# Optimization experiments

Hardware: AMD Instinct MI355X
Metric: run time of the kernel (lower is better)

## Reference

```python
import jax, jax.numpy as jnp
import numpy as np

B, N, D, H = 4, 2048, 1024, 64

def setup_inputs() -> dict:
    key = jax.random.key(0)
    ks = jax.random.split(key, 7)
    s = D ** -0.5  # torch Linear default init scale ~ U(-1/sqrt(fan_in), ...); scale randn similarly
    return {
        "x":  jax.random.normal(ks[0], (B, N, D), dtype=jnp.float32),
        "Wq": jax.random.normal(ks[1], (D, H), dtype=jnp.float32) * s,
        "bq": jax.random.normal(ks[2], (H,), dtype=jnp.float32) * s,
        "Wk": jax.random.normal(ks[3], (D, H), dtype=jnp.float32) * s,
        "bk": jax.random.normal(ks[4], (H,), dtype=jnp.float32) * s,
        "Wv": jax.random.normal(ks[5], (D, H), dtype=jnp.float32) * s,
        "bv": jax.random.normal(ks[6], (H,), dtype=jnp.float32) * s,
    }

def reference(x, Wq, bq, Wk, bk, Wv, bv):
    head_size = Wq.shape[1]
    q = x @ Wq + bq          # [B, N, H]
    k = x @ Wk + bk          # [B, N, H]
    v = x @ Wv + bv          # [B, N, H]
    scores = jnp.einsum("bid,bjd->bij", q, k)        # [B, N, N]
    # faithful to torch: keep upper triangle (col >= row), then mask exact zeros to -inf
    scores = jnp.triu(scores)
    scores = jnp.where(scores == 0, -jnp.inf, scores)
    attn = jax.nn.softmax(scores * (head_size ** -0.5), axis=-1)  # [B, N, N]
    # out = (V^T @ attn)^T  ==  attn^T @ V
    out = jnp.einsum("bji,bjh->bih", attn, v)         # [B, N, H]
    return out
```

## Files before the change

### kernel.cpp

```cpp
#include <hip/hip_runtime.h>
#include <math.h>

constexpr int kN = 2048;
constexpr int kD = 1024;

typedef __attribute__((ext_vector_type(8))) short bf16x8;
typedef __attribute__((ext_vector_type(4))) short bf16x4;
typedef __attribute__((ext_vector_type(4))) float f32x4;

#define MFMA(a, b, c) __builtin_amdgcn_mfma_f32_16x16x32_bf16(a, b, c, 0, 0, 0)

__device__ __forceinline__ short f2bf(float f) {
    unsigned u = __float_as_uint(f);
    u += 0x7fff + ((u >> 16) & 1);
    return (short)(u >> 16);
}
__device__ __forceinline__ float bf2f(short s) {
    return __uint_as_float(((unsigned)(unsigned short)s) << 16);
}

__device__ __forceinline__ void g2l(void* lds, const void* g, int nbytes, int t) {
    int lane = t & 63, w = t >> 6;
    for (int base = w * 1024; base < nbytes; base += 4096) {
        if (base + lane * 16 < nbytes) {
            __builtin_amdgcn_global_load_lds(
                (const __attribute__((address_space(1))) void*)((const char*)g + base + lane * 16),
                (__attribute__((address_space(3))) void*)((char*)lds + base),
                16, 0, 0);
        }
    }
}

__global__ __launch_bounds__(256) void prep_kernel(
        const float* __restrict__ Wq, const float* __restrict__ Wk,
        const float* __restrict__ Wv, const float* __restrict__ bq,
        const float* __restrict__ bk, const float* __restrict__ bv,
        short* __restrict__ Wt, float* __restrict__ bcat)
{
    int tid = blockIdx.x * 256 + threadIdx.x;
    int stride = gridDim.x * 256;
    for (int e = tid; e < 16 * 12 * 2 * 512; e += stride) {
        int kc = e / 12288;
        int rem = e - kc * 12288;
        int nt = rem >> 10;
        int r2 = rem & 1023;
        int f = r2 >> 9;
        int r3 = r2 & 511;
        int q8 = r3 >> 7;
        int l15 = (r3 >> 3) & 15;
        int el = r3 & 7;
        int n = nt * 16 + l15;
        int d = kc * 64 + f * 32 + q8 * 8 + el;
        float wv = (n < 64) ? Wq[d * 64 + n]
                 : (n < 128) ? Wk[d * 64 + (n - 64)]
                 : Wv[d * 64 + (n - 128)];
        Wt[e] = f2bf(wv);
    }
    if (tid < 192)
        bcat[tid] = (tid < 64) ? bq[tid] : (tid < 128) ? bk[tid - 64] : bv[tid - 128];
}

constexpr int XP = 1032;

__global__ __launch_bounds__(256) void qkv_kernel(
        const float* __restrict__ x, const short* __restrict__ Wt,
        const float* __restrict__ bcat,
        short* __restrict__ gq, short* __restrict__ gk, short* __restrict__ vt)
{
    __shared__ __align__(16) short xs[16 * XP];
    const int t = threadIdx.x;
    const int w = t >> 6, lane = t & 63, l15 = lane & 15, q8 = lane >> 4;
    const int m0 = blockIdx.x * 16;

    {
        int row = t >> 4, c4 = (t & 15) * 4;
        const float* xr = x + (size_t)(m0 + row) * kD;
        #pragma unroll
        for (int cc = 0; cc < 16; ++cc) {
            float4 xv = *(const float4*)&xr[cc * 64 + c4];
            bf16x4 pk = {f2bf(xv.x), f2bf(xv.y), f2bf(xv.z), f2bf(xv.w)};
            *(bf16x4*)&xs[row * XP + cc * 64 + c4] = pk;
        }
    }
    __syncthreads();

    f32x4 acc[3];
    #pragma unroll
    for (int ct = 0; ct < 3; ++ct) acc[ct] = (f32x4){0.f, 0.f, 0.f, 0.f};

    #pragma unroll 4
    for (int kc = 0; kc < 16; ++kc) {
        bf16x8 a0 = *(const bf16x8*)&xs[l15 * XP + kc * 64 + q8 * 8];
        bf16x8 a1 = *(const bf16x8*)&xs[l15 * XP + kc * 64 + 32 + q8 * 8];
        #pragma unroll
        for (int ct = 0; ct < 3; ++ct) {
            int nt = w * 3 + ct;
            const short* bp = Wt + ((size_t)(kc * 12 + nt) * 2) * 512 + lane * 8;
            bf16x8 b0 = *(const bf16x8*)bp;
            bf16x8 b1 = *(const bf16x8*)(bp + 512);
            acc[ct] = MFMA(a0, b0, acc[ct]);
            acc[ct] = MFMA(a1, b1, acc[ct]);
        }
    }

    const int bz = m0 >> 11;
    const int jt = (m0 & 2047) >> 6;
    const int jb = m0 & 63;
    #pragma unroll
    for (int ct = 0; ct < 3; ++ct) {
        int nb2 = w * 48 + ct * 16;
        int n = nb2 + l15;
        float bias = bcat[n];
        if (nb2 < 64) {
            #pragma unroll
            for (int r = 0; r < 4; ++r)
                gq[(size_t)(m0 + q8 * 4 + r) * 72 + n] = f2bf(acc[ct][r] + bias);
        } else if (nb2 < 128) {
            #pragma unroll
            for (int r = 0; r < 4; ++r)
                gk[(size_t)(m0 + q8 * 4 + r) * 72 + (n - 64)] = f2bf(acc[ct][r] + bias);
        } else {
            int h = n - 128;
            bf16x4 pk = {f2bf(acc[ct][0] + bias), f2bf(acc[ct][1] + bias),
                         f2bf(acc[ct][2] + bias), f2bf(acc[ct][3] + bias)};
            *(bf16x4*)&vt[((size_t)((bz * 32 + jt) * 64 + h)) * 72 + jb + q8 * 4] = pk;
        }
    }
}

__global__ __launch_bounds__(256) void stats_kernel(
        const short* __restrict__ gq, const short* __restrict__ gk,
        float* __restrict__ l2)
{
    __shared__ __align__(16) short qsm[64 * 72];
    __shared__ __align__(16) short ksm[2][64 * 72];
    const int t = threadIdx.x;
    const int w = t >> 6, lane = t & 63, l15 = lane & 15, q8 = lane >> 4;
    const int b = blockIdx.x;
    const int ic = b & 3, bz = (b >> 2) & 3, jt = b >> 4;
    const int j0 = jt * 64;
    const int ilo = ic * 512, ihi = ilo + 512;
    const int istart = (j0 > ilo) ? j0 : ilo;
    const int count = (istart < ihi) ? ((ihi - istart) >> 6) : 0;

    float lloc[4] = {0.f, 0.f, 0.f, 0.f};

    if (count > 0) {
        g2l(qsm, gq + (size_t)(bz * kN + j0) * 72, 64 * 144, t);
        g2l(ksm[0], gk + (size_t)(bz * kN + istart) * 72, 64 * 144, t);
        __syncthreads();
        int jrow = 16 * w + l15;
        bf16x8 a0 = *(const bf16x8*)&qsm[jrow * 72 + q8 * 8];
        bf16x8 a1 = *(const bf16x8*)&qsm[jrow * 72 + 32 + q8 * 8];

        for (int idx = 0; idx < count; ++idx) {
            const int cur = idx & 1;
            if (idx + 1 < count)
                g2l(ksm[cur ^ 1],
                    gk + (size_t)(bz * kN + istart + (idx + 1) * 64) * 72, 64 * 144, t);
            const int i0 = istart + idx * 64;
            #pragma unroll
            for (int it = 0; it < 4; ++it) {
                int irow = it * 16 + l15;
                bf16x8 b0 = *(const bf16x8*)&ksm[cur][irow * 72 + q8 * 8];
                bf16x8 b1 = *(const bf16x8*)&ksm[cur][irow * 72 + 32 + q8 * 8];
                f32x4 s = (f32x4){0.f, 0.f, 0.f, 0.f};
                s = MFMA(a0, b0, s);
                s = MFMA(a1, b1, s);
                int ig = i0 + it * 16 + l15;
                #pragma unroll
                for (int r = 0; r < 4; ++r) {
                    int jg = j0 + 16 * w + q8 * 4 + r;
                    float sv = s[r];
                    float e = __expf(sv * 0.125f);
                    lloc[r] += ((ig >= jg) && (sv != 0.0f)) ? e : 0.0f;
                }
            }
            __syncthreads();
        }
    }
    #pragma unroll
    for (int off = 1; off < 16; off <<= 1)
        #pragma unroll
        for (int r = 0; r < 4; ++r)
            lloc[r] += __shfl_xor(lloc[r], off);
    if (l15 == 0) {
        #pragma unroll
        for (int r = 0; r < 4; ++r)
            l2[ic * 8192 + bz * kN + j0 + 16 * w + q8 * 4 + r] = lloc[r];
    }
}

__global__ __launch_bounds__(256) void vscale_kernel(
        short* __restrict__ vt, const float* __restrict__ l2)
{
    __shared__ float rsm[64];
    const int g = blockIdx.x, t = threadIdx.x;
    if (t < 64) {
        int j = (g >> 5) * kN + (g & 31) * 64 + t;
        float l = l2[j] + l2[8192 + j] + l2[16384 + j] + l2[24576 + j];
        rsm[t] = (l > 0.f) ? 1.0f / l : 0.0f;
    }
    __syncthreads();
    const int h = t >> 2, c0 = (t & 3) * 16;
    size_t base = ((size_t)g * 64 + h) * 72 + c0;
    #pragma unroll
    for (int bb = 0; bb < 2; ++bb) {
        bf16x8 v = *(bf16x8*)&vt[base + bb * 8];
        bf16x8 o;
        #pragma unroll
        for (int e = 0; e < 8; ++e)
            o[e] = f2bf(bf2f(v[e]) * rsm[c0 + bb * 8 + e]);
        *(bf16x8*)&vt[base + bb * 8] = o;
    }
}

__global__ __launch_bounds__(256) void out_kernel(
        const short* __restrict__ gq, const short* __restrict__ gk,
        const short* __restrict__ vt, float* __restrict__ part)
{
    __shared__ __align__(16) short ksm[64 * 72];
    __shared__ __align__(16) short qsm[2][64 * 72];
    __shared__ __align__(16) short vsm[2][64 * 72];
    __shared__ __align__(16) short psm[64 * 72];
    const int t = threadIdx.x;
    const int w = t >> 6, lane = t & 63, l15 = lane & 15, q8 = lane >> 4;
    const int b = blockIdx.x;
    const int jc = b & 3, bz = (b >> 2) & 3, it = b >> 4;
    const int i0 = it * 64;
    const int jlo = jc * 512;
    const int jhi = (jlo + 512 < i0 + 64) ? (jlo + 512) : (i0 + 64);
    const int count = (jlo < jhi) ? ((jhi - jlo) >> 6) : 0;

    f32x4 oacc[4];
    #pragma unroll
    for (int i = 0; i < 4; ++i) oacc[i] = (f32x4){0.f, 0.f, 0.f, 0.f};

    if (count > 0) {
        g2l(ksm, gk + (size_t)(bz * kN + i0) * 72, 64 * 144, t);
        g2l(qsm[0], gq + (size_t)(bz * kN + jlo) * 72, 64 * 144, t);
        g2l(vsm[0], vt + (size_t)((bz * 32 + (jlo >> 6)) * 64) * 72, 64 * 144, t);
        __syncthreads();

        for (int idx = 0; idx < count; ++idx) {
            const int cur = idx & 1, nb = cur ^ 1;
            const int j0s = jlo + idx * 64;
            if (idx + 1 < count) {
                g2l(qsm[nb], gq + (size_t)(bz * kN + j0s + 64) * 72, 64 * 144, t);
                g2l(vsm[nb], vt + (size_t)((bz * 32 + ((j0s + 64) >> 6)) * 64) * 72,
                    64 * 144, t);
            }
            int jrow = 16 * w + l15;
            bf16x8 a0 = *(const bf16x8*)&qsm[cur][jrow * 72 + q8 * 8];
            bf16x8 a1 = *(const bf16x8*)&qsm[cur][jrow * 72 + 32 + q8 * 8];
            #pragma unroll
            for (int itile = 0; itile < 4; ++itile) {
                int irow = itile * 16 + l15;
                bf16x8 b0 = *(const bf16x8*)&ksm[irow * 72 + q8 * 8];
                bf16x8 b1 = *(const bf16x8*)&ksm[irow * 72 + 32 + q8 * 8];
                f32x4 sv4 = (f32x4){0.f, 0.f, 0.f, 0.f};
                sv4 = MFMA(a0, b0, sv4);
                sv4 = MFMA(a1, b1, sv4);
                int ig = i0 + itile * 16 + l15;
                bf16x4 pk;
                #pragma unroll
                for (int r = 0; r < 4; ++r) {
                    int jg = j0s + 16 * w + q8 * 4 + r;
                    float sv = sv4[r];
                    float p = ((ig >= jg) && (sv != 0.0f)) ? __expf(sv * 0.125f) : 0.0f;
                    pk[r] = f2bf(p);
                }
                *(bf16x4*)&psm[(itile * 16 + l15) * 72 + 16 * w + q8 * 4] = pk;
            }
            __syncthreads();

            bf16x8 pa0 = *(const bf16x8*)&psm[(16 * w + l15) * 72 + q8 * 8];
            bf16x8 pa1 = *(const bf16x8*)&psm[(16 * w + l15) * 72 + 32 + q8 * 8];
            #pragma unroll
            for (int ht = 0; ht < 4; ++ht) {
                int vrow = ht * 16 + l15;
                bf16x8 vb0 = *(const bf16x8*)&vsm[cur][vrow * 72 + q8 * 8];
                bf16x8 vb1 = *(const bf16x8*)&vsm[cur][vrow * 72 + 32 + q8 * 8];
                oacc[ht] = MFMA(pa0, vb0, oacc[ht]);
                oacc[ht] = MFMA(pa1, vb1, oacc[ht]);
            }
            __syncthreads();
        }
    }
    size_t base = ((size_t)(jc * 4 + bz) * kN + i0) * 64;
    #pragma unroll
    for (int ht = 0; ht < 4; ++ht)
        #pragma unroll
        for (int r = 0; r < 4; ++r)
            part[base + (size_t)(16 * w + q8 * 4 + r) * 64 + ht * 16 + l15] = oacc[ht][r];
}

__global__ __launch_bounds__(256) void reduce_kernel(
        const float* __restrict__ part, float* __restrict__ out)
{
    int idx = blockIdx.x * 256 + threadIdx.x;
    const float4* p = (const float4*)part;
    float4 a = p[idx];
    float4 b = p[idx + 131072];
    float4 c = p[idx + 262144];
    float4 d = p[idx + 393216];
    float4 r;
    r.x = a.x + b.x + c.x + d.x;
    r.y = a.y + b.y + c.y + d.y;
    r.z = a.z + b.z + c.z + d.z;
    r.w = a.w + b.w + c.w + d.w;
    ((float4*)out)[idx] = r;
}

extern "C" void kernel_launch(void* const* d_in, const int* in_sizes, int n_in,
                              void* d_out, int out_size, void* d_ws, size_t ws_size,
                              hipStream_t stream)
{
    const float* x  = (const float*)d_in[0];
    const float* Wq = (const float*)d_in[1];
    const float* bq = (const float*)d_in[2];
    const float* Wk = (const float*)d_in[3];
    const float* bk = (const float*)d_in[4];
    const float* Wv = (const float*)d_in[5];
    const float* bv = (const float*)d_in[6];
    float* out = (float*)d_out;

    char* base = (char*)d_ws;
    short* Wt   = (short*)(base);
    float* bcat = (float*)(base + 393216);
    short* gq   = (short*)(base + 394240);
    short* gk   = (short*)(base + 1573888);
    short* vt   = (short*)(base + 2753536);
    float* l2   = (float*)(base + 3933184);
    float* part = (float*)(base + 4064256);

    prep_kernel<<<256, 256, 0, stream>>>(Wq, Wk, Wv, bq, bk, bv, Wt, bcat);
    qkv_kernel<<<512, 256, 0, stream>>>(x, Wt, bcat, gq, gk, vt);
    stats_kernel<<<512, 256, 0, stream>>>(gq, gk, l2);
    vscale_kernel<<<128, 256, 0, stream>>>(vt, l2);
    out_kernel<<<512, 256, 0, stream>>>(gq, gk, vt, part);
    reduce_kernel<<<512, 256, 0, stream>>>(part, out);
}
```

Measured before the change: 126.3 us.

## Materialize exp scores in stats pass and reuse them in output pass

The stats kernel now writes the masked exponentiated scores as bf16 into a global buffer, laid out in MFMA-fragment order. The output kernel reads these fragments instead of recomputing QK^T and exp. V is stored in a fragment-friendly tiled layout so it can be loaded straight into registers without LDS or barriers. This removes the duplicated score MFMAs, exp work and LDS staging, but adds about 33 MB of global writes and reads for the P matrix.

```diff
diff --git a/kernel.cpp b/kernel.cpp
--- a/kernel.cpp
+++ b/kernel.cpp
@@ -120,17 +120,23 @@
             for (int r = 0; r < 4; ++r)
                 gk[(size_t)(m0 + q8 * 4 + r) * 72 + (n - 64)] = f2bf(acc[ct][r] + bias);
         } else {
-            int h = n - 128;
+            int ht = (nb2 - 128) >> 4;
+            int base_j = jb + q8 * 4;
+            int f = base_j >> 5;
+            int q8f = (base_j >> 3) & 3;
+            int e0 = base_j & 7;
             bf16x4 pk = {f2bf(acc[ct][0] + bias), f2bf(acc[ct][1] + bias),
                          f2bf(acc[ct][2] + bias), f2bf(acc[ct][3] + bias)};
-            *(bf16x4*)&vt[((size_t)((bz * 32 + jt) * 64 + h)) * 72 + jb + q8 * 4] = pk;
+            size_t addr = (((size_t)((bz * 32 + jt) * 4 + ht) * 2 + f) * 512)
+                          + (q8f * 16 + l15) * 8 + e0;
+            *(bf16x4*)&vt[addr] = pk;
         }
     }
 }
 
 __global__ __launch_bounds__(256) void stats_kernel(
         const short* __restrict__ gq, const short* __restrict__ gk,
-        float* __restrict__ l2)
+        float* __restrict__ l2, short* __restrict__ Pm)
 {
     __shared__ __align__(16) short qsm[64 * 72];
     __shared__ __align__(16) short ksm[2][64 * 72];
@@ -159,6 +165,8 @@
                 g2l(ksm[cur ^ 1],
                     gk + (size_t)(bz * kN + istart + (idx + 1) * 64) * 72, 64 * 144, t);
             const int i0 = istart + idx * 64;
+            const size_t tbase =
+                (((size_t)(bz * 32 + jt) * 32 + (size_t)(i0 >> 6)) * 4 + w) * 4 * 256;
             #pragma unroll
             for (int it = 0; it < 4; ++it) {
                 int irow = it * 16 + l15;
@@ -168,13 +176,17 @@
                 s = MFMA(a0, b0, s);
                 s = MFMA(a1, b1, s);
                 int ig = i0 + it * 16 + l15;
+                bf16x4 pk;
                 #pragma unroll
                 for (int r = 0; r < 4; ++r) {
                     int jg = j0 + 16 * w + q8 * 4 + r;
                     float sv = s[r];
                     float e = __expf(sv * 0.125f);
-                    lloc[r] += ((ig >= jg) && (sv != 0.0f)) ? e : 0.0f;
+                    bool valid = (ig >= jg) && (sv != 0.0f);
+                    lloc[r] += valid ? e : 0.0f;
+                    pk[r] = valid ? f2bf(e) : (short)0;
                 }
+                *(bf16x4*)&Pm[tbase + it * 256 + lane * 4] = pk;
             }
             __syncthreads();
         }
@@ -202,27 +214,29 @@
         rsm[t] = (l > 0.f) ? 1.0f / l : 0.0f;
     }
     __syncthreads();
-    const int h = t >> 2, c0 = (t & 3) * 16;
-    size_t base = ((size_t)g * 64 + h) * 72 + c0;
-    #pragma unroll
-    for (int bb = 0; bb < 2; ++bb) {
-        bf16x8 v = *(bf16x8*)&vt[base + bb * 8];
+    const int slice = t >> 5;
+    const int lane32 = t & 31;
+    const int f = slice & 1;
+    #pragma unroll
+    for (int half = 0; half < 2; ++half) {
+        int lidx = lane32 + half * 32;
+        int q8v = lidx >> 4;
+        size_t addr = ((size_t)g * 8 + slice) * 512 + lidx * 8;
+        bf16x8 v = *(bf16x8*)&vt[addr];
         bf16x8 o;
         #pragma unroll
-        for (int e = 0; e < 8; ++e)
-            o[e] = f2bf(bf2f(v[e]) * rsm[c0 + bb * 8 + e]);
-        *(bf16x8*)&vt[base + bb * 8] = o;
+        for (int e = 0; e < 8; ++e) {
+            int jl = f * 32 + q8v * 8 + e;
+            o[e] = f2bf(bf2f(v[e]) * rsm[jl]);
+        }
+        *(bf16x8*)&vt[addr] = o;
     }
 }
 
 __global__ __launch_bounds__(256) void out_kernel(
-        const short* __restrict__ gq, const short* __restrict__ gk,
-        const short* __restrict__ vt, float* __restrict__ part)
-{
-    __shared__ __align__(16) short ksm[64 * 72];
-    __shared__ __align__(16) short qsm[2][64 * 72];
-    __shared__ __align__(16) short vsm[2][64 * 72];
-    __shared__ __align__(16) short psm[64 * 72];
+        const short* __restrict__ Pm, const short* __restrict__ vt,
+        float* __restrict__ part)
+{
     const int t = threadIdx.x;
     const int w = t >> 6, lane = t & 63, l15 = lane & 15, q8 = lane >> 4;
     const int b = blockIdx.x;
@@ -236,55 +250,26 @@
     #pragma unroll
     for (int i = 0; i < 4; ++i) oacc[i] = (f32x4){0.f, 0.f, 0.f, 0.f};
 
-    if (count > 0) {
-        g2l(ksm, gk + (size_t)(bz * kN + i0) * 72, 64 * 144, t);
-        g2l(qsm[0], gq + (size_t)(bz * kN + jlo) * 72, 64 * 144, t);
-        g2l(vsm[0], vt + (size_t)((bz * 32 + (jlo >> 6)) * 64) * 72, 64 * 144, t);
-        __syncthreads();
-
-        for (int idx = 0; idx < count; ++idx) {
-            const int cur = idx & 1, nb = cur ^ 1;
-            const int j0s = jlo + idx * 64;
-            if (idx + 1 < count) {
-                g2l(qsm[nb], gq + (size_t)(bz * kN + j0s + 64) * 72, 64 * 144, t);
-                g2l(vsm[nb], vt + (size_t)((bz * 32 + ((j0s + 64) >> 6)) * 64) * 72,
-                    64 * 144, t);
-            }
-            int jrow = 16 * w + l15;
-            bf16x8 a0 = *(const bf16x8*)&qsm[cur][jrow * 72 + q8 * 8];
-            bf16x8 a1 = *(const bf16x8*)&qsm[cur][jrow * 72 + 32 + q8 * 8];
-            #pragma unroll
-            for (int itile = 0; itile < 4; ++itile) {
-                int irow = itile * 16 + l15;
-                bf16x8 b0 = *(const bf16x8*)&ksm[irow * 72 + q8 * 8];
-                bf16x8 b1 = *(const bf16x8*)&ksm[irow * 72 + 32 + q8 * 8];
-                f32x4 sv4 = (f32x4){0.f, 0.f, 0.f, 0.f};
-                sv4 = MFMA(a0, b0, sv4);
-                sv4 = MFMA(a1, b1, sv4);
-                int ig = i0 + itile * 16 + l15;
-                bf16x4 pk;
-                #pragma unroll
-                for (int r = 0; r < 4; ++r) {
-                    int jg = j0s + 16 * w + q8 * 4 + r;
-                    float sv = sv4[r];
-                    float p = ((ig >= jg) && (sv != 0.0f)) ? __expf(sv * 0.125f) : 0.0f;
-                    pk[r] = f2bf(p);
-                }
-                *(bf16x4*)&psm[(itile * 16 + l15) * 72 + 16 * w + q8 * 4] = pk;
-            }
-            __syncthreads();
-
-            bf16x8 pa0 = *(const bf16x8*)&psm[(16 * w + l15) * 72 + q8 * 8];
-            bf16x8 pa1 = *(const bf16x8*)&psm[(16 * w + l15) * 72 + 32 + q8 * 8];
-            #pragma unroll
-            for (int ht = 0; ht < 4; ++ht) {
-                int vrow = ht * 16 + l15;
-                bf16x8 vb0 = *(const bf16x8*)&vsm[cur][vrow * 72 + q8 * 8];
-                bf16x8 vb1 = *(const bf16x8*)&vsm[cur][vrow * 72 + 32 + q8 * 8];
-                oacc[ht] = MFMA(pa0, vb0, oacc[ht]);
-                oacc[ht] = MFMA(pa1, vb1, oacc[ht]);
-            }
-            __syncthreads();
+    const int aoff = ((q8 >> 1) * 4 + w) * 256 + (q8 & 1) * 128 + l15 * 4;
+
+    for (int idx = 0; idx < count; ++idx) {
+        const int jt = (jlo >> 6) + idx;
+        const size_t tb = ((size_t)(bz * 32 + jt) * 32 + it) * 16 * 256;
+        const short* pa = Pm + tb + aoff;
+        bf16x4 a00 = *(const bf16x4*)pa;
+        bf16x4 a01 = *(const bf16x4*)(pa + 64);
+        bf16x4 a10 = *(const bf16x4*)(pa + 2048);
+        bf16x4 a11 = *(const bf16x4*)(pa + 2048 + 64);
+        bf16x8 a0 = {a00[0], a00[1], a00[2], a00[3], a01[0], a01[1], a01[2], a01[3]};
+        bf16x8 a1 = {a10[0], a10[1], a10[2], a10[3], a11[0], a11[1], a11[2], a11[3]};
+
+        const short* vb = vt + (size_t)(bz * 32 + jt) * 8 * 512 + lane * 8;
+        #pragma unroll
+        for (int ht = 0; ht < 4; ++ht) {
+            bf16x8 b0 = *(const bf16x8*)(vb + (ht * 2 + 0) * 512);
+            bf16x8 b1 = *(const bf16x8*)(vb + (ht * 2 + 1) * 512);
+            oacc[ht] = MFMA(a0, b0, oacc[ht]);
+            oacc[ht] = MFMA(a1, b1, oacc[ht]);
         }
     }
     size_t base = ((size_t)(jc * 4 + bz) * kN + i0) * 64;
@@ -331,13 +316,14 @@
     short* gq   = (short*)(base + 394240);
     short* gk   = (short*)(base + 1573888);
     short* vt   = (short*)(base + 2753536);
-    float* l2   = (float*)(base + 3933184);
-    float* part = (float*)(base + 4064256);
+    float* l2   = (float*)(base + 3802112);
+    short* Pm   = (short*)(base + 3933184);
+    float* part = (float*)(base + 37487616);
 
     prep_kernel<<<256, 256, 0, stream>>>(Wq, Wk, Wv, bq, bk, bv, Wt, bcat);
     qkv_kernel<<<512, 256, 0, stream>>>(x, Wt, bcat, gq, gk, vt);
-    stats_kernel<<<512, 256, 0, stream>>>(gq, gk, l2);
+    stats_kernel<<<512, 256, 0, stream>>>(gq, gk, l2, Pm);
     vscale_kernel<<<128, 256, 0, stream>>>(vt, l2);
-    out_kernel<<<512, 256, 0, stream>>>(gq, gk, vt, part);
+    out_kernel<<<512, 256, 0, stream>>>(Pm, vt, part);
     reduce_kernel<<<512, 256, 0, stream>>>(part, out);
 }
```

Measured after the change: 127.7 us. About the same (+1.1%).

## Fold V normalization into out_kernel and replace partial reduce with atomics

Applied to the files above, without the earlier changes.

Removes the separate vscale kernel by computing reciprocal column sums in out_kernel and applying them to the probabilities before the PV matmul. Drops the partial-sum buffer and reduce kernel: the output is zeroed in prep_kernel and each j-chunk block atomically adds its contribution. This cuts two launches and the partial-buffer round trip. In exchange it adds float atomics, which make the summation order nondeterministic, and a small per-tile l2 load.

```diff
diff --git a/kernel.cpp b/kernel.cpp
--- a/kernel.cpp
+++ b/kernel.cpp
@@ -14,9 +14,6 @@
     unsigned u = __float_as_uint(f);
     u += 0x7fff + ((u >> 16) & 1);
     return (short)(u >> 16);
-}
-__device__ __forceinline__ float bf2f(short s) {
-    return __uint_as_float(((unsigned)(unsigned short)s) << 16);
 }
 
 __device__ __forceinline__ void g2l(void* lds, const void* g, int nbytes, int t) {
@@ -35,10 +32,13 @@
         const float* __restrict__ Wq, const float* __restrict__ Wk,
         const float* __restrict__ Wv, const float* __restrict__ bq,
         const float* __restrict__ bk, const float* __restrict__ bv,
-        short* __restrict__ Wt, float* __restrict__ bcat)
+        short* __restrict__ Wt, float* __restrict__ bcat,
+        float* __restrict__ out)
 {
     int tid = blockIdx.x * 256 + threadIdx.x;
     int stride = gridDim.x * 256;
+    for (int e = tid; e < 131072; e += stride)
+        ((float4*)out)[e] = make_float4(0.f, 0.f, 0.f, 0.f);
     for (int e = tid; e < 16 * 12 * 2 * 512; e += stride) {
         int kc = e / 12288;
         int rem = e - kc * 12288;
@@ -191,38 +191,16 @@
     }
 }
 
-__global__ __launch_bounds__(256) void vscale_kernel(
-        short* __restrict__ vt, const float* __restrict__ l2)
-{
-    __shared__ float rsm[64];
-    const int g = blockIdx.x, t = threadIdx.x;
-    if (t < 64) {
-        int j = (g >> 5) * kN + (g & 31) * 64 + t;
-        float l = l2[j] + l2[8192 + j] + l2[16384 + j] + l2[24576 + j];
-        rsm[t] = (l > 0.f) ? 1.0f / l : 0.0f;
-    }
-    __syncthreads();
-    const int h = t >> 2, c0 = (t & 3) * 16;
-    size_t base = ((size_t)g * 64 + h) * 72 + c0;
-    #pragma unroll
-    for (int bb = 0; bb < 2; ++bb) {
-        bf16x8 v = *(bf16x8*)&vt[base + bb * 8];
-        bf16x8 o;
-        #pragma unroll
-        for (int e = 0; e < 8; ++e)
-            o[e] = f2bf(bf2f(v[e]) * rsm[c0 + bb * 8 + e]);
-        *(bf16x8*)&vt[base + bb * 8] = o;
-    }
-}
-
 __global__ __launch_bounds__(256) void out_kernel(
         const short* __restrict__ gq, const short* __restrict__ gk,
-        const short* __restrict__ vt, float* __restrict__ part)
+        const short* __restrict__ vt, const float* __restrict__ l2,
+        float* __restrict__ out)
 {
     __shared__ __align__(16) short ksm[64 * 72];
     __shared__ __align__(16) short qsm[2][64 * 72];
     __shared__ __align__(16) short vsm[2][64 * 72];
     __shared__ __align__(16) short psm[64 * 72];
+    __shared__ float rsm[2][64];
     const int t = threadIdx.x;
     const int w = t >> 6, lane = t & 63, l15 = lane & 15, q8 = lane >> 4;
     const int b = blockIdx.x;
@@ -232,84 +210,81 @@
     const int jhi = (jlo + 512 < i0 + 64) ? (jlo + 512) : (i0 + 64);
     const int count = (jlo < jhi) ? ((jhi - jlo) >> 6) : 0;
 
+    if (count <= 0) return;
+
     f32x4 oacc[4];
     #pragma unroll
     for (int i = 0; i < 4; ++i) oacc[i] = (f32x4){0.f, 0.f, 0.f, 0.f};
 
-    if (count > 0) {
-        g2l(ksm, gk + (size_t)(bz * kN + i0) * 72, 64 * 144, t);
-        g2l(qsm[0], gq + (size_t)(bz * kN + jlo) * 72, 64 * 144, t);
-        g2l(vsm[0], vt + (size_t)((bz * 32 + (jlo >> 6)) * 64) * 72, 64 * 144, t);
+    g2l(ksm, gk + (size_t)(bz * kN + i0) * 72, 64 * 144, t);
+    g2l(qsm[0], gq + (size_t)(bz * kN + jlo) * 72, 64 * 144, t);
+    g2l(vsm[0], vt + (size_t)((bz * 32 + (jlo >> 6)) * 64) * 72, 64 * 144, t);
+    if (t < 64) {
+        int j = bz * kN + jlo + t;
+        float l = l2[j] + l2[8192 + j] + l2[16384 + j] + l2[24576 + j];
+        rsm[0][t] = (l > 0.f) ? 1.0f / l : 0.0f;
+    }
+    __syncthreads();
+
+    for (int idx = 0; idx < count; ++idx) {
+        const int cur = idx & 1, nb = cur ^ 1;
+        const int j0s = jlo + idx * 64;
+        if (idx + 1 < count) {
+            g2l(qsm[nb], gq + (size_t)(bz * kN + j0s + 64) * 72, 64 * 144, t);
+            g2l(vsm[nb], vt + (size_t)((bz * 32 + ((j0s + 64) >> 6)) * 64) * 72,
+                64 * 144, t);
+            if (t < 64) {
+                int j = bz * kN + j0s + 64 + t;
+                float l = l2[j] + l2[8192 + j] + l2[16384 + j] + l2[24576 + j];
+                rsm[nb][t] = (l > 0.f) ? 1.0f / l : 0.0f;
+            }
+        }
+        int jrow = 16 * w + l15;
+        bf16x8 a0 = *(const bf16x8*)&qsm[cur][jrow * 72 + q8 * 8];
+        bf16x8 a1 = *(const bf16x8*)&qsm[cur][jrow * 72 + 32 + q8 * 8];
+        #pragma unroll
+        for (int itile = 0; itile < 4; ++itile) {
+            int irow = itile * 16 + l15;
+            bf16x8 b0 = *(const bf16x8*)&ksm[irow * 72 + q8 * 8];
+            bf16x8 b1 = *(const bf16x8*)&ksm[irow * 72 + 32 + q8 * 8];
+            f32x4 sv4 = (f32x4){0.f, 0.f, 0.f, 0.f};
+            sv4 = MFMA(a0, b0, sv4);
+            sv4 = MFMA(a1, b1, sv4);
+            int ig = i0 + itile * 16 + l15;
+            bf16x4 pk;
+            #pragma unroll
+            for (int r = 0; r < 4; ++r) {
+                int jl = 16 * w + q8 * 4 + r;
+                int jg = j0s + jl;
+                float sv = sv4[r];
+                float p = ((ig >= jg) && (sv != 0.0f))
+                        ? __expf(sv * 0.125f) * rsm[cur][jl] : 0.0f;
+                pk[r] = f2bf(p);
+            }
+            *(bf16x4*)&psm[(itile * 16 + l15) * 72 + 16 * w + q8 * 4] = pk;
+        }
         __syncthreads();
 
-        for (int idx = 0; idx < count; ++idx) {
-            const int cur = idx & 1, nb = cur ^ 1;
-            const int j0s = jlo + idx * 64;
-            if (idx + 1 < count) {
-                g2l(qsm[nb], gq + (size_t)(bz * kN + j0s + 64) * 72, 64 * 144, t);
-                g2l(vsm[nb], vt + (size_t)((bz * 32 + ((j0s + 64) >> 6)) * 64) * 72,
-                    64 * 144, t);
-            }
-            int jrow = 16 * w + l15;
-            bf16x8 a0 = *(const bf16x8*)&qsm[cur][jrow * 72 + q8 * 8];
-            bf16x8 a1 = *(const bf16x8*)&qsm[cur][jrow * 72 + 32 + q8 * 8];
-            #pragma unroll
-            for (int itile = 0; itile < 4; ++itile) {
-                int irow = itile * 16 + l15;
-                bf16x8 b0 = *(const bf16x8*)&ksm[irow * 72 + q8 * 8];
-                bf16x8 b1 = *(const bf16x8*)&ksm[irow * 72 + 32 + q8 * 8];
-                f32x4 sv4 = (f32x4){0.f, 0.f, 0.f, 0.f};
-                sv4 = MFMA(a0, b0, sv4);
-                sv4 = MFMA(a1, b1, sv4);
-                int ig = i0 + itile * 16 + l15;
-                bf16x4 pk;
-                #pragma unroll
-                for (int r = 0; r < 4; ++r) {
-                    int jg = j0s + 16 * w + q8 * 4 + r;
-                    float sv = sv4[r];
-                    float p = ((ig >= jg) && (sv != 0.0f)) ? __expf(sv * 0.125f) : 0.0f;
-                    pk[r] = f2bf(p);
-                }
-                *(bf16x4*)&psm[(itile * 16 + l15) * 72 + 16 * w + q8 * 4] = pk;
-            }
-            __syncthreads();
-
-            bf16x8 pa0 = *(const bf16x8*)&psm[(16 * w + l15) * 72 + q8 * 8];
-            bf16x8 pa1 = *(const bf16x8*)&psm[(16 * w + l15) * 72 + 32 + q8 * 8];
-            #pragma unroll
-            for (int ht = 0; ht < 4; ++ht) {
-                int vrow = ht * 16 + l15;
-                bf16x8 vb0 = *(const bf16x8*)&vsm[cur][vrow * 72 + q8 * 8];
-                bf16x8 vb1 = *(const bf16x8*)&vsm[cur][vrow * 72 + 32 + q8 * 8];
-                oacc[ht] = MFMA(pa0, vb0, oacc[ht]);
-                oacc[ht] = MFMA(pa1, vb1, oacc[ht]);
-            }
-            __syncthreads();
-        }
-    }
-    size_t base = ((size_t)(jc * 4 + bz) * kN + i0) * 64;
+        bf16x8 pa0 = *(const bf16x8*)&psm[(16 * w + l15) * 72 + q8 * 8];
+        bf16x8 pa1 = *(const bf16x8*)&psm[(16 * w + l15) * 72 + 32 + q8 * 8];
+        #pragma unroll
+        for (int ht = 0; ht < 4; ++ht) {
+            int vrow = ht * 16 + l15;
+            bf16x8 vb0 = *(const bf16x8*)&vsm[cur][vrow * 72 + q8 * 8];
+            bf16x8 vb1 = *(const bf16x8*)&vsm[cur][vrow * 72 + 32 + q8 * 8];
+            oacc[ht] = MFMA(pa0, vb0, oacc[ht]);
+            oacc[ht] = MFMA(pa1, vb1, oacc[ht]);
+        }
+        __syncthreads();
+    }
+
+    size_t base = ((size_t)(bz * kN + i0)) * 64;
     #pragma unroll
     for (int ht = 0; ht < 4; ++ht)
         #pragma unroll
         for (int r = 0; r < 4; ++r)
-            part[base + (size_t)(16 * w + q8 * 4 + r) * 64 + ht * 16 + l15] = oacc[ht][r];
-}
-
-__global__ __launch_bounds__(256) void reduce_kernel(
-        const float* __restrict__ part, float* __restrict__ out)
-{
-    int idx = blockIdx.x * 256 + threadIdx.x;
-    const float4* p = (const float4*)part;
-    float4 a = p[idx];
-    float4 b = p[idx + 131072];
-    float4 c = p[idx + 262144];
-    float4 d = p[idx + 393216];
-    float4 r;
-    r.x = a.x + b.x + c.x + d.x;
-    r.y = a.y + b.y + c.y + d.y;
-    r.z = a.z + b.z + c.z + d.z;
-    r.w = a.w + b.w + c.w + d.w;
-    ((float4*)out)[idx] = r;
+            atomicAdd(&out[base + (size_t)(16 * w + q8 * 4 + r) * 64 + ht * 16 + l15],
+                      oacc[ht][r]);
 }
 
 extern "C" void kernel_launch(void* const* d_in, const int* in_sizes, int n_in,
@@ -332,12 +307,9 @@
     short* gk   = (short*)(base + 1573888);
     short* vt   = (short*)(base + 2753536);
     float* l2   = (float*)(base + 3933184);
-    float* part = (float*)(base + 4064256);
-
-    prep_kernel<<<256, 256, 0, stream>>>(Wq, Wk, Wv, bq, bk, bv, Wt, bcat);
+
+    prep_kernel<<<256, 256, 0, stream>>>(Wq, Wk, Wv, bq, bk, bv, Wt, bcat, out);
     qkv_kernel<<<512, 256, 0, stream>>>(x, Wt, bcat, gq, gk, vt);
     stats_kernel<<<512, 256, 0, stream>>>(gq, gk, l2);
-    vscale_kernel<<<128, 256, 0, stream>>>(vt, l2);
-    out_kernel<<<512, 256, 0, stream>>>(gq, gk, vt, part);
-    reduce_kernel<<<512, 256, 0, stream>>>(part, out);
-}
+    out_kernel<<<512, 256, 0, stream>>>(gq, gk, vt, l2, out);
+}
```

Result: no change. 126.7 us (+0.3%).
